# Kernel optimization log

Measured on AMD Instinct MI355X. Metric: run time of the kernel, lower is better.

The kernel has to match this reference:

```python
import jax, jax.numpy as jnp
import numpy as np

N = 20000      # nodes
D_IN = 512     # input_dim
D_H = 256      # hyper_dim = input_dim // 2
C = 7          # class_num
E = 320000     # edges per class graph
E2 = 100000    # candidate pair list length
B = 8192       # batch of evaluated pairs (edge_id)
H3 = D_IN + C * D_H  # 2304, GatedNetwork / fc2 width
MIN = 1e-15
CURV = 1.0

def _norm(x):
    return jnp.maximum(jnp.linalg.norm(x, axis=-1, keepdims=True), MIN)

def artanh(x):
    x = jnp.clip(x, -1.0 + 1e-7, 1.0 - 1e-7)
    return 0.5 * (jnp.log1p(x) - jnp.log1p(-x))

def proj(x, c):
    # clip to inside the Poincare ball
    n = _norm(x)
    maxn = (1.0 - 4e-3) / jnp.sqrt(c)
    return jnp.where(n > maxn, x / n * maxn, x)

def expmap0(u, c):
    sc = jnp.sqrt(c); n = _norm(u)
    return jnp.tanh(sc * n) * u / (sc * n)

def logmap0(p, c):
    sc = jnp.sqrt(c); n = _norm(p)
    return artanh(sc * n) * p / (sc * n)

def mobius_add(x, y, c):
    x2 = jnp.sum(x * x, -1, keepdims=True)
    y2 = jnp.sum(y * y, -1, keepdims=True)
    xy = jnp.sum(x * y, -1, keepdims=True)
    num = (1 + 2 * c * xy + c * y2) * x + (1 - c * x2) * y
    den = 1 + 2 * c * xy + c * c * x2 * y2
    return num / jnp.maximum(den, MIN)

def mobius_matvec(m, x, c):
    sc = jnp.sqrt(c)
    xn = _norm(x)
    mx = x @ m.T
    mxn = _norm(mx)
    res = jnp.tanh(mxn / xn * artanh(sc * xn)) * mx / (mxn * sc)
    zero = jnp.all(mx == 0, axis=-1, keepdims=True)
    return jnp.where(zero, jnp.zeros((), mx.dtype), res)


def setup_inputs() -> dict:
    key = jax.random.key(0)
    ks = iter(jax.random.split(key, 48))
    def dense(shape, fan_in):
        return jax.random.normal(next(ks), shape, jnp.float32) * (1.0 / np.sqrt(fan_in))
    inp = {}
    inp['f1'] = jax.random.normal(next(ks), (N, D_IN), jnp.float32)
    inp['adj_src'] = jax.random.randint(next(ks), (C, E), 0, N)
    inp['adj_dst'] = jax.random.randint(next(ks), (C, E), 0, N)
    inp['adj_val'] = jax.random.uniform(next(ks), (C, E), jnp.float32) / 16.0  # ~row-normalized weights
    inp['edge_src'] = jax.random.randint(next(ks), (C, E), 0, N)
    inp['edge_dst'] = jax.random.randint(next(ks), (C, E), 0, N)
    inp['edge_index'] = jax.random.randint(next(ks), (2, E2), 0, N)
    inp['edge_id'] = jax.random.randint(next(ks), (B,), 0, E2)
    # per-class HypLinear
    inp['W_hyp'] = dense((C, D_H, D_IN), D_IN)
    inp['b_hyp'] = jnp.zeros((C, D_H), jnp.float32)
    # per-class HyperbolicDecoder linear
    inp['Wd'] = dense((C, D_H, D_H), D_H)
    inp['bd'] = jnp.zeros((C, D_H), jnp.float32)
    # per-class GIN MLP: lin1 -> BN -> tanh -> lin2
    inp['Wg1'] = dense((C, D_H, D_H), D_H)
    inp['bg1'] = jnp.zeros((C, D_H), jnp.float32)
    inp['gamma'] = jnp.ones((C, D_H), jnp.float32)
    inp['beta'] = jnp.zeros((C, D_H), jnp.float32)
    inp['Wg2'] = dense((C, D_H, D_H), D_H)
    inp['bg2'] = jnp.zeros((C, D_H), jnp.float32)
    # GatedInteractionNetwork
    inp['Wgate'] = dense((H3, H3), H3); inp['bgate'] = jnp.zeros((H3,), jnp.float32)
    inp['Wint'] = dense((H3, H3), H3); inp['bint'] = jnp.zeros((H3,), jnp.float32)
    inp['Wout'] = dense((H3, H3), H3); inp['bout'] = jnp.zeros((H3,), jnp.float32)
    # fc2 MLP head
    inp['Wf1'] = dense((H3 // 2, H3), H3); inp['bf1'] = jnp.zeros((H3 // 2,), jnp.float32)
    inp['Wf2'] = dense((H3 // 4, H3 // 2), H3 // 2); inp['bf2'] = jnp.zeros((H3 // 4,), jnp.float32)
    inp['Wf3'] = dense((C, H3 // 4), H3 // 4); inp['bf3'] = jnp.zeros((C,), jnp.float32)
    return inp


def reference(f1, adj_val, W_hyp, b_hyp, Wd, bd, Wg1, bg1, gamma, beta, Wg2, bg2,
              Wgate, bgate, Wint, bint, Wout, bout, Wf1, bf1, Wf2, bf2, Wf3, bf3,
              adj_src, adj_dst, edge_src, edge_dst, edge_index, edge_id):
    c = jnp.float32(CURV)
    # proj_tan0 is identity on the Poincare ball
    x_hyp = proj(expmap0(f1, c), c)
    outs = [f1]
    for i in range(C):
        # HypLinear: mobius matvec + hyperbolic bias
        res = proj(mobius_matvec(W_hyp[i], x_hyp, c), c)
        hb = proj(expmap0(b_hyp[i][None, :], c), c)
        res = proj(mobius_add(res, hb, c), c)
        # HypAgg: spmm(adj, logmap0(x)) then expmap0
        xt = logmap0(res, c)                     # [N, D_H]
        msg = adj_val[i][:, None] * xt[adj_src[i]]
        support = jax.ops.segment_sum(msg, adj_dst[i], num_segments=N)
        h = proj(expmap0(support, c), c)
        # HypAct: relu in tangent space at origin
        h = proj(expmap0(jax.nn.relu(logmap0(h, c)), c), c)
        # HyperbolicDecoder: logmap0 then euclidean linear
        d = logmap0(h, c) @ Wd[i].T + bd[i]
        # GIN (1 layer, eps=0): mlp(x + sum_neighbors x_j), mlp = lin->BN->tanh->lin
        agg = d + jax.ops.segment_sum(d[edge_src[i]], edge_dst[i], num_segments=N)
        z = agg @ Wg1[i].T + bg1[i]
        mu = jnp.mean(z, axis=0)
        var = jnp.var(z, axis=0)
        z = (z - mu) / jnp.sqrt(var + 1e-5) * gamma[i] + beta[i]
        z = jnp.tanh(z)
        outs.append(z @ Wg2[i].T + bg2[i])
    x = jnp.concatenate(outs, axis=1)            # [N, H3]
    nid = edge_index[:, edge_id]                 # [2, B]
    x1 = x[nid[0]]
    x2 = x[nid[1]]
    # GatedInteractionNetwork
    gate = jax.nn.sigmoid((x1 + x2) @ Wgate.T + bgate)
    gi = gate * jax.nn.relu((x1 * x2) @ Wint.T + bint)
    g = gi @ Wout.T + bout
    # fc2 head
    h1 = jax.nn.relu(g @ Wf1.T + bf1)
    h2 = jax.nn.relu(h1 @ Wf2.T + bf2)
    return h2 @ Wf3.T + bf3                      # [B, C]
```

## Files before the change

### kernel.cpp

```cpp
#include <hip/hip_runtime.h>
#include <math.h>

#define N_NODES 20000
#define D_INN   512
#define DH      256
#define NCH     7
#define NE      320000
#define NE2     100000
#define NB      8192
#define H3      2304
#define MAXN    0.996f
#define LOG2E   1.44269504f

typedef unsigned short u16;
typedef __attribute__((ext_vector_type(8))) short bf16x8;
typedef __attribute__((ext_vector_type(4))) float f32x4;

__device__ __forceinline__ u16 f2b(float f) {
    unsigned int x = __float_as_uint(f);
    unsigned int r = (x + 0x7fffu + ((x >> 16) & 1u)) >> 16;
    return (u16)r;
}
__device__ __forceinline__ float b2f(u16 u) {
    return __uint_as_float(((unsigned int)u) << 16);
}
__device__ __forceinline__ float blo(unsigned int u) { return __uint_as_float(u << 16); }
__device__ __forceinline__ float bhi(unsigned int u) { return __uint_as_float(u & 0xffff0000u); }
__device__ __forceinline__ unsigned int pk2(float a, float b) {
    return (unsigned int)f2b(a) | ((unsigned int)f2b(b) << 16);
}

__device__ __forceinline__ float rcp_f(float x) { return __builtin_amdgcn_rcpf(x); }
__device__ __forceinline__ float exp2_f(float x) { return __builtin_amdgcn_exp2f(x); }
__device__ __forceinline__ float log2_f(float x) { return __builtin_amdgcn_logf(x); }
__device__ __forceinline__ float tanh_fast(float x) {
    float xc = fminf(fmaxf(x, -15.f), 15.f);
    float t = exp2_f(xc * (2.f * LOG2E));
    return (t - 1.f) * rcp_f(t + 1.f);
}
__device__ __forceinline__ float artanh_fast(float x) {
    x = fminf(fmaxf(x, -1.0f + 1e-7f), 1.0f - 1e-7f);
    return 0.34657359f * log2_f((1.f + x) * rcp_f(1.f - x));
}
__device__ __forceinline__ float sigmoid_fast(float x) {
    return rcp_f(1.f + exp2_f(-x * LOG2E));
}

__device__ __forceinline__ float wave_sum(float v) {
    #pragma unroll
    for (int off = 32; off > 0; off >>= 1) v += __shfl_xor(v, off, 64);
    return v;
}

__device__ __forceinline__ float block_sum256(float v) {
    __shared__ float sred[4];
    #pragma unroll
    for (int off = 32; off > 0; off >>= 1) v += __shfl_down(v, off, 64);
    int lane = threadIdx.x & 63;
    int w = threadIdx.x >> 6;
    if (lane == 0) sred[w] = v;
    __syncthreads();
    float tot = sred[0] + sred[1] + sred[2] + sred[3];
    __syncthreads();
    return tot;
}

__global__ void k_zero(float* __restrict__ p, int n) {
    int i = blockIdx.x * 256 + threadIdx.x;
    if (i < n) p[i] = 0.0f;
}
__global__ void k_izero(int* __restrict__ p, int n) {
    int i = blockIdx.x * 256 + threadIdx.x;
    if (i < n) p[i] = 0;
}

__global__ void k_f2b(const float* __restrict__ s, u16* __restrict__ d, int n4) {
    int i = blockIdx.x * 256 + threadIdx.x;
    int stride = gridDim.x * 256;
    for (; i < n4; i += stride) {
        float4 v = ((const float4*)s)[i];
        uint2 o; o.x = pk2(v.x, v.y); o.y = pk2(v.z, v.w);
        ((uint2*)d)[i] = o;
    }
}

__global__ void k_bias2(const float* __restrict__ a, const float* __restrict__ b,
                        float* __restrict__ o) {
    int i = blockIdx.x * 256 + threadIdx.x;
    if (i < H3) o[i] = a[i];
    else if (i < 2 * H3) o[i] = b[i - H3];
}

__global__ void k_gi(const u16* __restrict__ gate, const u16* __restrict__ tmp,
                     u16* __restrict__ out, int total4) {
    int i = blockIdx.x * 256 + threadIdx.x;
    int stride = gridDim.x * 256;
    for (; i < total4; i += stride) {
        uint2 g = ((const uint2*)gate)[i];
        uint2 t = ((const uint2*)tmp)[i];
        uint2 o;
        o.x = pk2(blo(g.x) * fmaxf(blo(t.x), 0.f), bhi(g.x) * fmaxf(bhi(t.x), 0.f));
        o.y = pk2(blo(g.y) * fmaxf(blo(t.y), 0.f), bhi(g.y) * fmaxf(bhi(t.y), 0.f));
        ((uint2*)out)[i] = o;
    }
}

__global__ void k_twd(const float* __restrict__ Wd, u16* __restrict__ Wdt) {
    __shared__ float tile[16][17];
    int z = blockIdx.z;
    int bx = blockIdx.x * 16, by = blockIdx.y * 16;
    int tx = threadIdx.x & 15, ty = threadIdx.x >> 4;
    tile[ty][tx] = Wd[(size_t)z * DH * DH + (size_t)(by + ty) * DH + bx + tx];
    __syncthreads();
    Wdt[(size_t)z * DH * DH + (size_t)(bx + ty) * DH + by + tx] = f2b(tile[tx][ty]);
}

__global__ void k_tr(const float* __restrict__ Win, u16* __restrict__ Wt) {
    __shared__ float tile[16][17];
    int bx = blockIdx.x * 16, by = blockIdx.y * 16;
    int tx = threadIdx.x & 15, ty = threadIdx.x >> 4;
    tile[ty][tx] = Win[(size_t)(by + ty) * H3 + bx + tx];
    __syncthreads();
    Wt[(size_t)(bx + ty) * H3 + by + tx] = f2b(tile[tx][ty]);
}

__global__ void k_bvec(const float* __restrict__ Wf1, const float* __restrict__ bout,
                       const float* __restrict__ bf1, float* __restrict__ bcomb) {
    int r = blockIdx.x * 4 + (threadIdx.x >> 6);
    int lane = threadIdx.x & 63;
    const float* row = Wf1 + (size_t)r * H3;
    float s = 0.f;
    for (int j = lane; j < H3; j += 64) s = fmaf(row[j], bout[j], s);
    s = wave_sum(s);
    if (lane == 0) bcomb[r] = s + bf1[r];
}

__global__ void k_cvec(const float* __restrict__ Wg1, const float* __restrict__ bd,
                       float* __restrict__ cvec) {
    int z = blockIdx.x, j = threadIdx.x;
    const float* row = Wg1 + (size_t)z * DH * DH + (size_t)j * DH;
    const float* b = bd + (size_t)z * DH;
    float s = 0.f;
    for (int k = 0; k < DH; ++k) s = fmaf(row[k], b[k], s);
    cvec[(size_t)z * DH + j] = s;
}

__global__ void k_hist2(const int* __restrict__ adjd, const int* __restrict__ edged,
                        int* __restrict__ cnt, int G) {
    int z = blockIdx.y;
    const int* dst = (z < G) ? adjd + (size_t)z * NE : edged + (size_t)(z - G) * NE;
    cnt += (size_t)z * N_NODES;
    int i = blockIdx.x * 256 + threadIdx.x;
    if (i < NE) atomicAdd(&cnt[dst[i]], 1);
}

__global__ void k_scan(int* __restrict__ cnt, int* __restrict__ rowptr) {
    int z = blockIdx.x;
    cnt += (size_t)z * N_NODES;
    rowptr += (size_t)z * (N_NODES + 1);
    __shared__ int part[256];
    int t = threadIdx.x;
    const int CH = (N_NODES + 255) / 256;
    int beg = t * CH;
    int end = beg + CH; if (end > N_NODES) end = N_NODES;
    int s = 0;
    for (int i = beg; i < end; ++i) s += cnt[i];
    part[t] = s;
    __syncthreads();
    for (int off = 1; off < 256; off <<= 1) {
        int v = (t >= off) ? part[t - off] : 0;
        __syncthreads();
        part[t] += v;
        __syncthreads();
    }
    int run = (t == 0) ? 0 : part[t - 1];
    for (int i = beg; i < end; ++i) {
        int c = cnt[i];
        rowptr[i] = run;
        cnt[i] = run;
        run += c;
    }
    if (t == 255) rowptr[N_NODES] = part[255];
}

__global__ void k_place2(const int* __restrict__ adjs, const int* __restrict__ adjd,
                         const float* __restrict__ adjv, const int* __restrict__ edges,
                         const int* __restrict__ edged, int* __restrict__ cursor,
                         uint2* __restrict__ padj, int* __restrict__ psrcE, int G) {
    int z = blockIdx.y;
    bool isadj = z < G;
    const int* src = isadj ? adjs + (size_t)z * NE : edges + (size_t)(z - G) * NE;
    const int* dst = isadj ? adjd + (size_t)z * NE : edged + (size_t)(z - G) * NE;
    cursor += (size_t)z * N_NODES;
    int i = blockIdx.x * 256 + threadIdx.x;
    if (i < NE) {
        int d = dst[i];
        int pos = atomicAdd(&cursor[d], 1);
        if (isadj) {
            uint2 p;
            p.x = (unsigned int)src[i];
            p.y = __float_as_uint(adjv[(size_t)z * NE + i]);
            padj[(size_t)z * NE + pos] = p;
        } else {
            psrcE[(size_t)(z - G) * NE + pos] = src[i];
        }
    }
}

__global__ void k_expmap_proj_in(const float* __restrict__ f1,
                                 u16* __restrict__ xhyp, float* __restrict__ xhn) {
    int r = blockIdx.x, t = threadIdx.x;
    const float* u = f1 + (size_t)r * D_INN;
    float v0 = u[t], v1 = u[t + 256];
    float ss = block_sum256(v0 * v0 + v1 * v1);
    float nraw = sqrtf(ss);
    float n = fmaxf(nraw, 1e-15f);
    float c = tanh_fast(n) * rcp_f(n);
    float ny = c * nraw;
    float np = fmaxf(ny, 1e-15f);
    float s = (np > MAXN) ? MAXN * rcp_f(np) : 1.0f;
    float cs = c * s;
    u16* o = xhyp + (size_t)r * D_INN;
    o[t] = f2b(cs * v0);
    o[t + 256] = f2b(cs * v1);
    if (t == 0) xhn[r] = fminf(np, MAXN);
}

__global__ void k_hb(const float* __restrict__ b_hyp,
                     float* __restrict__ hb, float* __restrict__ hb2) {
    int i = blockIdx.x, t = threadIdx.x;
    float v = b_hyp[i * DH + t];
    float ss = block_sum256(v * v);
    float nraw = sqrtf(ss);
    float n = fmaxf(nraw, 1e-15f);
    float c = tanh_fast(n) * rcp_f(n);
    float ny = c * nraw;
    float np = fmaxf(ny, 1e-15f);
    float s = (np > MAXN) ? MAXN * rcp_f(np) : 1.0f;
    float hv = c * s * v;
    hb[i * DH + t] = hv;
    float s2 = block_sum256(hv * hv);
    if (t == 0) hb2[i] = s2;
}

__global__ void k_rowfuse1(u16* __restrict__ T, const float* __restrict__ xhn,
                           const float* __restrict__ hb, const float* __restrict__ hb2) {
    int z = blockIdx.y;
    int n = blockIdx.x * 4 + (threadIdx.x >> 6);
    int lane = threadIdx.x & 63;
    u16* row = T + ((size_t)z * N_NODES + n) * DH;
    const float* hbz = hb + (size_t)z * DH;
    uint2 u = *(const uint2*)(row + lane * 4);
    float m0 = blo(u.x), m1 = bhi(u.x), m2 = blo(u.y), m3 = bhi(u.y);
    float ss = wave_sum(m0 * m0 + m1 * m1 + m2 * m2 + m3 * m3);
    float mxn_raw = sqrtf(ss);
    float mxn = fmaxf(mxn_raw, 1e-15f);
    float xn = xhn[n];
    float tt = tanh_fast(mxn * rcp_f(xn) * artanh_fast(xn));
    float coef = tt * rcp_f(mxn);
    float nres = coef * mxn_raw;
    float np = fmaxf(nres, 1e-15f);
    float s1 = (np > MAXN) ? MAXN * rcp_f(np) : 1.0f;
    float cs = coef * s1;
    float r0 = cs * m0, r1 = cs * m1, r2 = cs * m2, r3 = cs * m3;
    float n1 = fminf(np, MAXN);
    float4 hv = *(const float4*)(hbz + lane * 4);
    float xy = wave_sum(r0 * hv.x + r1 * hv.y + r2 * hv.z + r3 * hv.w);
    float x2 = n1 * n1, y2 = hb2[z];
    float ca = 1.0f + 2.0f * xy + y2;
    float cb = 1.0f - x2;
    float rden = rcp_f(fmaxf(1.0f + 2.0f * xy + x2 * y2, 1e-15f));
    float o0 = (ca * r0 + cb * hv.x) * rden;
    float o1 = (ca * r1 + cb * hv.y) * rden;
    float o2 = (ca * r2 + cb * hv.z) * rden;
    float o3 = (ca * r3 + cb * hv.w) * rden;
    float no2 = wave_sum(o0 * o0 + o1 * o1 + o2 * o2 + o3 * o3);
    float nop = fmaxf(sqrtf(no2), 1e-15f);
    float s2 = (nop > MAXN) ? MAXN * rcp_f(nop) : 1.0f;
    float n2 = fminf(nop, MAXN);
    float fin = artanh_fast(n2) * rcp_f(n2) * s2;
    uint2 o; o.x = pk2(fin * o0, fin * o1); o.y = pk2(fin * o2, fin * o3);
    *(uint2*)(row + lane * 4) = o;
}

__global__ void k_gather_fuse2(const int* __restrict__ rowptr, const uint2* __restrict__ padj,
                               const u16* __restrict__ xt, u16* __restrict__ out) {
    int z = blockIdx.y;
    rowptr += (size_t)z * (N_NODES + 1);
    padj += (size_t)z * NE;
    xt += (size_t)z * N_NODES * DH;
    out += (size_t)z * N_NODES * DH;
    int n = blockIdx.x * 4 + (threadIdx.x >> 6);
    int lane = threadIdx.x & 63;
    int beg = rowptr[n], end = rowptr[n + 1];
    float a0 = 0.f, a1 = 0.f, a2 = 0.f, a3 = 0.f;
    float b0 = 0.f, b1 = 0.f, b2 = 0.f, b3 = 0.f;
    int i = beg;
    for (; i + 2 <= end; i += 2) {
        uint2 p0 = padj[i];
        uint2 p1 = padj[i + 1];
        uint2 x0 = *(const uint2*)(xt + (size_t)p0.x * DH + lane * 4);
        uint2 x1 = *(const uint2*)(xt + (size_t)p1.x * DH + lane * 4);
        float v0 = __uint_as_float(p0.y), v1 = __uint_as_float(p1.y);
        a0 = fmaf(v0, blo(x0.x), a0);
        a1 = fmaf(v0, bhi(x0.x), a1);
        a2 = fmaf(v0, blo(x0.y), a2);
        a3 = fmaf(v0, bhi(x0.y), a3);
        b0 = fmaf(v1, blo(x1.x), b0);
        b1 = fmaf(v1, bhi(x1.x), b1);
        b2 = fmaf(v1, blo(x1.y), b2);
        b3 = fmaf(v1, bhi(x1.y), b3);
    }
    if (i < end) {
        uint2 p = padj[i];
        uint2 x0 = *(const uint2*)(xt + (size_t)p.x * DH + lane * 4);
        float v = __uint_as_float(p.y);
        a0 = fmaf(v, blo(x0.x), a0);
        a1 = fmaf(v, bhi(x0.x), a1);
        a2 = fmaf(v, blo(x0.y), a2);
        a3 = fmaf(v, bhi(x0.y), a3);
    }
    a0 += b0; a1 += b1; a2 += b2; a3 += b3;
    float ss = wave_sum(a0 * a0 + a1 * a1 + a2 * a2 + a3 * a3);
    float nraw = sqrtf(ss);
    float n_ = fmaxf(nraw, 1e-15f);
    float c1 = tanh_fast(n_) * rcp_f(n_);
    float nh = c1 * nraw;
    float np1 = fmaxf(nh, 1e-15f);
    float s1 = (np1 > MAXN) ? MAXN * rcp_f(np1) : 1.0f;
    float n1 = fminf(np1, MAXN);
    float cu = artanh_fast(n1) * rcp_f(n1) * s1 * c1;
    float u0 = fmaxf(cu * a0, 0.f), u1 = fmaxf(cu * a1, 0.f);
    float u2 = fmaxf(cu * a2, 0.f), u3 = fmaxf(cu * a3, 0.f);
    float ss2 = wave_sum(u0 * u0 + u1 * u1 + u2 * u2 + u3 * u3);
    float n2raw = sqrtf(ss2);
    float n2 = fmaxf(n2raw, 1e-15f);
    float c3 = tanh_fast(n2) * rcp_f(n2);
    float ne = c3 * n2raw;
    float np3 = fmaxf(ne, 1e-15f);
    float s3 = (np3 > MAXN) ? MAXN * rcp_f(np3) : 1.0f;
    float n3 = fminf(np3, MAXN);
    float cf = artanh_fast(n3) * rcp_f(n3) * s3 * c3;
    uint2 o; o.x = pk2(cf * u0, cf * u1); o.y = pk2(cf * u2, cf * u3);
    *(uint2*)(out + (size_t)n * DH + lane * 4) = o;
}

__global__ void k_gather_add(const int* __restrict__ rowptr, const int* __restrict__ psrc,
                             const u16* __restrict__ d, u16* __restrict__ out) {
    int z = blockIdx.y;
    rowptr += (size_t)z * (N_NODES + 1);
    psrc += (size_t)z * NE;
    d += (size_t)z * N_NODES * DH;
    out += (size_t)z * N_NODES * DH;
    int n = blockIdx.x * 4 + (threadIdx.x >> 6);
    int lane = threadIdx.x & 63;
    int beg = rowptr[n], end = rowptr[n + 1];
    uint2 u0v = *(const uint2*)(d + (size_t)n * DH + lane * 4);
    float a0 = blo(u0v.x), a1 = bhi(u0v.x), a2 = blo(u0v.y), a3 = bhi(u0v.y);
    float b0 = 0.f, b1 = 0.f, b2 = 0.f, b3 = 0.f;
    int i = beg;
    for (; i + 2 <= end; i += 2) {
        int s0 = psrc[i], s1 = psrc[i + 1];
        uint2 x0 = *(const uint2*)(d + (size_t)s0 * DH + lane * 4);
        uint2 x1 = *(const uint2*)(d + (size_t)s1 * DH + lane * 4);
        a0 += blo(x0.x); a1 += bhi(x0.x); a2 += blo(x0.y); a3 += bhi(x0.y);
        b0 += blo(x1.x); b1 += bhi(x1.x); b2 += blo(x1.y); b3 += bhi(x1.y);
    }
    if (i < end) {
        int s0 = psrc[i];
        uint2 x0 = *(const uint2*)(d + (size_t)s0 * DH + lane * 4);
        a0 += blo(x0.x); a1 += bhi(x0.x); a2 += blo(x0.y); a3 += bhi(x0.y);
    }
    a0 += b0; a1 += b1; a2 += b2; a3 += b3;
    uint2 o; o.x = pk2(a0, a1); o.y = pk2(a2, a3);
    *(uint2*)(out + (size_t)n * DH + lane * 4) = o;
}

__global__ void k_colstats(const u16* __restrict__ zp,
                           float* __restrict__ csum, float* __restrict__ csq) {
    int z = blockIdx.y;
    zp += (size_t)z * N_NODES * DH;
    csum += (size_t)z * DH;
    csq += (size_t)z * DH;
    int t = threadIdx.x;
    int r0 = blockIdx.x * 100;
    float s = 0.0f, q = 0.0f;
    for (int r = r0; r < r0 + 100; ++r) {
        float v = b2f(zp[(size_t)r * DH + t]);
        s += v;
        q += v * v;
    }
    atomicAdd(&csum[t], s);
    atomicAdd(&csq[t], q);
}

__global__ void k_normtanh_v(u16* __restrict__ zp, const float* __restrict__ csum,
                             const float* __restrict__ csq, const float* __restrict__ gamma,
                             const float* __restrict__ beta, int total4) {
    const float inv_n = 1.0f / N_NODES;
    int i = blockIdx.x * 256 + threadIdx.x;
    int stride = gridDim.x * 256;
    for (; i < total4; i += stride) {
        int e0 = i * 4;
        int z = e0 / (N_NODES * DH);
        int j0 = e0 & (DH - 1);
        int zb = z * DH + j0;
        uint2 u = ((uint2*)zp)[i];
        float v[4] = {blo(u.x), bhi(u.x), blo(u.y), bhi(u.y)};
        #pragma unroll
        for (int k = 0; k < 4; ++k) {
            float mu = csum[zb + k] * inv_n;
            float var = csq[zb + k] * inv_n - mu * mu;
            float inv = __builtin_amdgcn_rsqf(var + 1e-5f);
            v[k] = tanh_fast((v[k] - mu) * inv * gamma[zb + k] + beta[zb + k]);
        }
        uint2 o; o.x = pk2(v[0], v[1]); o.y = pk2(v[2], v[3]);
        ((uint2*)zp)[i] = o;
    }
}

__global__ void k_pair0(const int* __restrict__ ei, const int* __restrict__ eid,
                        const float* __restrict__ f1, u16* __restrict__ S,
                        u16* __restrict__ P) {
    int b = blockIdx.x, t = threadIdx.x;
    int e = eid[b];
    int n0 = ei[e], n1 = ei[NE2 + e];
    float2 a = *(const float2*)(f1 + (size_t)n0 * D_INN + t * 2);
    float2 c = *(const float2*)(f1 + (size_t)n1 * D_INN + t * 2);
    ((unsigned int*)(S + (size_t)b * H3))[t] = pk2(a.x + c.x, a.y + c.y);
    ((unsigned int*)(P + (size_t)b * H3))[t] = pk2(a.x * c.x, a.y * c.y);
}

__global__ void k_gather_ch(const int* __restrict__ ei, const int* __restrict__ eid,
                            const u16* __restrict__ zch, u16* __restrict__ S,
                            u16* __restrict__ P, int col0base) {
    int z = blockIdx.y;
    const u16* zp = zch + (size_t)z * N_NODES * DH;
    int col0 = col0base + z * DH;
    int b = blockIdx.x * 4 + (threadIdx.x >> 6);
    int lane = threadIdx.x & 63;
    int e = eid[b];
    int n0 = ei[e], n1 = ei[NE2 + e];
    uint2 ua = *(const uint2*)(zp + (size_t)n0 * DH + lane * 4);
    uint2 ub = *(const uint2*)(zp + (size_t)n1 * DH + lane * 4);
    float a0 = blo(ua.x), a1 = bhi(ua.x), a2 = blo(ua.y), a3 = bhi(ua.y);
    float c0 = blo(ub.x), c1 = bhi(ub.x), c2 = blo(ub.y), c3 = bhi(ub.y);
    uint2 so; so.x = pk2(a0 + c0, a1 + c1); so.y = pk2(a2 + c2, a3 + c3);
    uint2 po; po.x = pk2(a0 * c0, a1 * c1); po.y = pk2(a2 * c2, a3 * c3);
    *(uint2*)(S + (size_t)b * H3 + col0 + lane * 4) = so;
    *(uint2*)(P + (size_t)b * H3 + col0 + lane * 4) = po;
}

__global__ void k_final(const u16* __restrict__ h2, const float* __restrict__ Wf3,
                        const float* __restrict__ bf3, float* __restrict__ out) {
    int r = blockIdx.x, t = threadIdx.x;
    const u16* hr = h2 + (size_t)r * 576;
    float acc[7] = {0, 0, 0, 0, 0, 0, 0};
    for (int cb = t; cb < 576; cb += 64) {
        float h = b2f(hr[cb]);
        #pragma unroll
        for (int o = 0; o < 7; ++o) acc[o] = fmaf(h, Wf3[o * 576 + cb], acc[o]);
    }
    #pragma unroll
    for (int o = 0; o < 7; ++o) {
        #pragma unroll
        for (int off = 32; off > 0; off >>= 1) acc[o] += __shfl_down(acc[o], off, 64);
    }
    if (t == 0) {
        #pragma unroll
        for (int o = 0; o < 7; ++o) out[(size_t)r * 7 + o] = acc[o] + bf3[o];
    }
}

template <int EP>
__global__ __launch_bounds__(256, 2) void k_gemm_mfma(
    const u16* __restrict__ A, const u16* __restrict__ W,
    const float* __restrict__ bias, void* __restrict__ outv,
    const int* __restrict__ rpe, const float* __restrict__ cvec,
    int M, int N, int K, size_t sA, size_t sW, size_t sC, int sBias) {
    __shared__ short As[8192];
    __shared__ short Ws[8192];
    const int gx = gridDim.x, gy = gridDim.y;
    const int plane = gx * gy;
    const int total = plane * gridDim.z;
    const int orig = (blockIdx.z * gy + blockIdx.y) * gx + blockIdx.x;
    const int q8 = total >> 3, r8 = total & 7, xcd = orig & 7;
    const int wg = (xcd < r8 ? xcd * (q8 + 1) : r8 * (q8 + 1) + (xcd - r8) * q8) + (orig >> 3);
    const int z = wg / plane;
    const int rem = wg - z * plane;
    const int row0 = (rem / gx) * 128, col0 = (rem % gx) * 128;
    A += (size_t)z * sA;
    W += (size_t)z * sW;
    const size_t zC = (size_t)z * sC;
    const int* rp = (EP == 7) ? rpe + (size_t)z * (N_NODES + 1) : nullptr;
    const float* cv = (EP == 7) ? cvec + (size_t)z * DH : nullptr;
    const int t = threadIdx.x;
    const int lane = t & 63;
    const int w = t >> 6;
    const int wr = w >> 1, wc = w & 1;
    const int sr8 = lane >> 3;
    const int csrc = (lane & 7) ^ sr8;
    int gr[4], gc[4];
    #pragma unroll
    for (int p = 0; p < 4; ++p) {
        int rb = w + p * 4;
        gr[p] = row0 + rb * 8 + sr8; if (gr[p] >= M) gr[p] = M - 1;
        gc[p] = col0 + rb * 8 + sr8; if (gc[p] >= N) gc[p] = N - 1;
    }
    const int fr = lane & 15, fq4 = lane >> 4;
    f32x4 acc[4][4] = {};
    for (int k0 = 0; k0 < K; k0 += 64) {
        #pragma unroll
        for (int p = 0; p < 4; ++p) {
            int rb = w + p * 4;
            __builtin_amdgcn_global_load_lds(
                (const __attribute__((address_space(1))) unsigned int*)(A + (size_t)gr[p] * K + k0 + csrc * 8),
                (__attribute__((address_space(3))) unsigned int*)(As + rb * 512), 16, 0, 0);
            __builtin_amdgcn_global_load_lds(
                (const __attribute__((address_space(1))) unsigned int*)(W + (size_t)gc[p] * K + k0 + csrc * 8),
                (__attribute__((address_space(3))) unsigned int*)(Ws + rb * 512), 16, 0, 0);
        }
        __syncthreads();
        bf16x8 af[4][2], bfr[4][2];
        #pragma unroll
        for (int m = 0; m < 4; ++m) {
            int ar = wr * 64 + m * 16 + fr;
            #pragma unroll
            for (int kk = 0; kk < 2; ++kk) {
                int q = kk * 4 + fq4;
                af[m][kk] = *(const bf16x8*)(As + ar * 64 + ((q ^ (ar & 7)) * 8));
            }
        }
        #pragma unroll
        for (int n = 0; n < 4; ++n) {
            int br = wc * 64 + n * 16 + fr;
            #pragma unroll
            for (int kk = 0; kk < 2; ++kk) {
                int q = kk * 4 + fq4;
                bfr[n][kk] = *(const bf16x8*)(Ws + br * 64 + ((q ^ (br & 7)) * 8));
            }
        }
        #pragma unroll
        for (int m = 0; m < 4; ++m)
            #pragma unroll
            for (int n = 0; n < 4; ++n)
                #pragma unroll
                for (int kk = 0; kk < 2; ++kk)
                    acc[m][n] = __builtin_amdgcn_mfma_f32_16x16x32_bf16(
                        af[m][kk], bfr[n][kk], acc[m][n], 0, 0, 0);
        __syncthreads();
    }
    const int cl = lane & 15, rh = (lane >> 4) * 4;
    #pragma unroll
    for (int m = 0; m < 4; ++m) {
        float indf[4];
        if (EP == 7) {
            #pragma unroll
            for (int r = 0; r < 4; ++r) {
                int row = row0 + wr * 64 + m * 16 + rh + r;
                if (row >= M) row = M - 1;
                indf[r] = 1.0f + (float)(rp[row + 1] - rp[row]);
            }
        }
        #pragma unroll
        for (int n = 0; n < 4; ++n) {
            int col = col0 + wc * 64 + n * 16 + cl;
            if (col >= N) continue;
            float bv = bias ? bias[z * sBias + col] : 0.0f;
            float cvc = (EP == 7) ? cv[col] : 0.0f;
            #pragma unroll
            for (int r = 0; r < 4; ++r) {
                int row = row0 + wr * 64 + m * 16 + rh + r;
                if (row >= M) continue;
                float v = acc[m][n][r] + bv;
                size_t idx = zC + (size_t)row * N + col;
                if (EP == 2) ((u16*)outv)[idx] = f2b(sigmoid_fast(v));
                if (EP == 3) ((u16*)outv)[idx] = f2b(fmaxf(v, 0.0f));
                if (EP == 5) ((u16*)outv)[idx] = f2b(v);
                if (EP == 6) ((float*)outv)[idx] = fmaxf(v, 0.0f);
                if (EP == 7) ((u16*)outv)[idx] = f2b(v + indf[r] * cvc);
                if (EP == 8) ((u16*)outv)[idx] = (z == 0) ? f2b(sigmoid_fast(v)) : f2b(v);
            }
        }
    }
}

static inline void gemm_b(int ep, const u16* A, const u16* W, const float* bias, void* out,
                          const int* rpe, const float* cvec,
                          int M, int N, int K, int Z,
                          size_t sA, size_t sW, size_t sC, int sBias, hipStream_t st) {
    dim3 g((N + 127) / 128, (M + 127) / 128, Z);
    switch (ep) {
        case 2: k_gemm_mfma<2><<<g, 256, 0, st>>>(A, W, bias, out, rpe, cvec, M, N, K, sA, sW, sC, sBias); break;
        case 3: k_gemm_mfma<3><<<g, 256, 0, st>>>(A, W, bias, out, rpe, cvec, M, N, K, sA, sW, sC, sBias); break;
        case 5: k_gemm_mfma<5><<<g, 256, 0, st>>>(A, W, bias, out, rpe, cvec, M, N, K, sA, sW, sC, sBias); break;
        case 6: k_gemm_mfma<6><<<g, 256, 0, st>>>(A, W, bias, out, rpe, cvec, M, N, K, sA, sW, sC, sBias); break;
        case 7: k_gemm_mfma<7><<<g, 256, 0, st>>>(A, W, bias, out, rpe, cvec, M, N, K, sA, sW, sC, sBias); break;
        case 8: k_gemm_mfma<8><<<g, 256, 0, st>>>(A, W, bias, out, rpe, cvec, M, N, K, sA, sW, sC, sBias); break;
    }
}

static inline void conv_w(const float* s, u16* d, size_t n, hipStream_t st) {
    int n4 = (int)(n / 4);
    int grid = (n4 + 255) / 256;
    if (grid > 2048) grid = 2048;
    k_f2b<<<grid, 256, 0, st>>>(s, d, n4);
}

extern "C" void kernel_launch(void* const* d_in, const int* in_sizes, int n_in, void* d_out,
                              int out_size, void* d_ws, size_t ws_size, hipStream_t stream) {
    const float* f1 = (const float*)d_in[0];
    const int* adj_src = (const int*)d_in[1];
    const int* adj_dst = (const int*)d_in[2];
    const float* adj_val = (const float*)d_in[3];
    const int* edge_src = (const int*)d_in[4];
    const int* edge_dst = (const int*)d_in[5];
    const int* edge_index = (const int*)d_in[6];
    const int* edge_id = (const int*)d_in[7];
    const float* W_hyp = (const float*)d_in[8];
    const float* b_hyp = (const float*)d_in[9];
    const float* Wd = (const float*)d_in[10];
    const float* bd = (const float*)d_in[11];
    const float* Wg1 = (const float*)d_in[12];
    const float* bg1 = (const float*)d_in[13];
    const float* gamma = (const float*)d_in[14];
    const float* beta = (const float*)d_in[15];
    const float* Wg2 = (const float*)d_in[16];
    const float* bg2 = (const float*)d_in[17];
    const float* Wgate = (const float*)d_in[18];
    const float* bgate = (const float*)d_in[19];
    const float* Wint = (const float*)d_in[20];
    const float* bint = (const float*)d_in[21];
    const float* Wout = (const float*)d_in[22];
    const float* bout = (const float*)d_in[23];
    const float* Wf1 = (const float*)d_in[24];
    const float* bf1 = (const float*)d_in[25];
    const float* Wf2 = (const float*)d_in[26];
    const float* bf2 = (const float*)d_in[27];
    const float* Wf3 = (const float*)d_in[28];
    const float* bf3 = (const float*)d_in[29];
    float* outp = (float*)d_out;

    const bool single = ws_size >= 253400000ull;
    const int ngroups = single ? 1 : 2;
    const int GM = single ? 7 : 4;
    int g0s[2] = {0, 4};
    int gns[2] = {GM, 3};

    char* base = (char*)d_ws;
    size_t off = 0;
    auto alloc = [&](size_t bytes) -> char* {
        char* p = base + off;
        off += (bytes + 255) & ~(size_t)255;
        return p;
    };
    u16* Whyp_b = (u16*)alloc((size_t)NCH * DH * D_INN * 2);
    u16* Wc_b   = (u16*)alloc((size_t)NCH * DH * DH * 2);
    u16* Wg1_b  = (u16*)alloc((size_t)NCH * DH * DH * 2);
    u16* Wg2_b  = (u16*)alloc((size_t)NCH * DH * DH * 2);
    u16* Wgate_b = (u16*)alloc((size_t)H3 * H3 * 2);
    u16* Wint_b  = (u16*)alloc((size_t)H3 * H3 * 2);
    u16* Wcomb_b = (u16*)alloc((size_t)1152 * H3 * 2);
    u16* Wf2_b   = (u16*)alloc((size_t)576 * 1152 * 2);
    u16* S_b = (u16*)alloc((size_t)NB * H3 * 2);
    u16* P_b = (u16*)alloc((size_t)NB * H3 * 2);
    const size_t NDB = (size_t)N_NODES * DH;
    u16* buf1 = (u16*)alloc((size_t)GM * NDB * 2);
    u16* buf2 = (u16*)alloc((size_t)GM * NDB * 2);
    u16* xhyp_b = single ? buf2 : (u16*)alloc((size_t)N_NODES * D_INN * 2);
    int* cntC; int* rowptrC; uint2* padjC; int* psrcE;
    if (single) {
        padjC = (uint2*)S_b;
        psrcE = (int*)((char*)S_b + (size_t)GM * NE * 8);
        cntC = (int*)P_b;
        rowptrC = (int*)((char*)P_b + (size_t)2 * GM * N_NODES * 4);
    } else {
        cntC = (int*)alloc((size_t)2 * GM * N_NODES * 4);
        rowptrC = (int*)alloc((size_t)2 * GM * (N_NODES + 1) * 4);
        padjC = (uint2*)alloc((size_t)GM * NE * 8);
        psrcE = (int*)alloc((size_t)GM * NE * 4);
    }
    float* xhn = (float*)alloc((size_t)N_NODES * 4);
    float* hb = (float*)alloc((size_t)NCH * DH * 4);
    float* hb2 = (float*)alloc(NCH * 4);
    float* csum = (float*)alloc((size_t)GM * DH * 4);
    float* csq = (float*)alloc((size_t)GM * DH * 4);
    float* cvec_d = (float*)alloc((size_t)NCH * DH * 4);
    float* bias2 = (float*)alloc((size_t)2 * H3 * 4);
    float* bcomb = (float*)alloc((size_t)1152 * 4);
    u16* WoutT_b = buf1;
    u16* Wf1_b = buf1 + (size_t)H3 * H3;
    u16* Wdt_b = Wf1_b + (size_t)1152 * H3;
    u16* GT = buf1;
    u16* h2b = buf2;

    const int EG = (NE + 255) / 256;

    conv_w(W_hyp, Whyp_b, (size_t)NCH * DH * D_INN, stream);
    conv_w(Wg1, Wg1_b, (size_t)NCH * DH * DH, stream);
    conv_w(Wg2, Wg2_b, (size_t)NCH * DH * DH, stream);
    conv_w(Wgate, Wgate_b, (size_t)H3 * H3, stream);
    conv_w(Wint, Wint_b, (size_t)H3 * H3, stream);
    conv_w(Wf1, Wf1_b, (size_t)1152 * H3, stream);
    conv_w(Wf2, Wf2_b, (size_t)576 * 1152, stream);
    k_bias2<<<(2 * H3 + 255) / 256, 256, 0, stream>>>(bgate, bint, bias2);
    k_twd<<<dim3(16, 16, NCH), 256, 0, stream>>>(Wd, Wdt_b);
    gemm_b(5, Wg1_b, Wdt_b, nullptr, Wc_b, nullptr, nullptr,
           DH, DH, DH, NCH, (size_t)DH * DH, (size_t)DH * DH, (size_t)DH * DH, 0, stream);
    k_cvec<<<NCH, 256, 0, stream>>>(Wg1, bd, cvec_d);
    k_tr<<<dim3(144, 144), 256, 0, stream>>>(Wout, WoutT_b);
    gemm_b(5, Wf1_b, WoutT_b, nullptr, Wcomb_b, nullptr, nullptr,
           1152, H3, H3, 1, 0, 0, 0, 0, stream);
    k_bvec<<<1152 / 4, 256, 0, stream>>>(Wf1, bout, bf1, bcomb);

    k_expmap_proj_in<<<N_NODES, 256, 0, stream>>>(f1, xhyp_b, xhn);
    k_hb<<<NCH, 256, 0, stream>>>(b_hyp, hb, hb2);
    if (!single) k_pair0<<<NB, 256, 0, stream>>>(edge_index, edge_id, f1, S_b, P_b);

    for (int gi = 0; gi < ngroups; ++gi) {
        const int g0 = g0s[gi], G = gns[gi];
        const size_t eoff = (size_t)g0 * NE;
        const int G2 = 2 * G;
        const int* rpE = rowptrC + (size_t)G * (N_NODES + 1);
        k_izero<<<(G2 * N_NODES + 255) / 256, 256, 0, stream>>>(cntC, G2 * N_NODES);
        k_hist2<<<dim3(EG, G2), 256, 0, stream>>>(adj_dst + eoff, edge_dst + eoff, cntC, G);
        k_scan<<<G2, 256, 0, stream>>>(cntC, rowptrC);
        k_place2<<<dim3(EG, G2), 256, 0, stream>>>(adj_src + eoff, adj_dst + eoff,
                                                   adj_val + eoff, edge_src + eoff,
                                                   edge_dst + eoff, cntC, padjC, psrcE, G);
        gemm_b(5, xhyp_b, Whyp_b + (size_t)g0 * DH * D_INN, nullptr, buf1, nullptr,
               nullptr, N_NODES, DH, D_INN, G, 0, (size_t)DH * D_INN, NDB, 0, stream);
        k_rowfuse1<<<dim3(N_NODES / 4, G), 256, 0, stream>>>(buf1, xhn, hb + g0 * DH, hb2 + g0);
        k_gather_fuse2<<<dim3(N_NODES / 4, G), 256, 0, stream>>>(rowptrC, padjC, buf1, buf2);
        k_gather_add<<<dim3(N_NODES / 4, G), 256, 0, stream>>>(rpE, psrcE, buf2, buf1);
        gemm_b(7, buf1, Wc_b + (size_t)g0 * DH * DH, bg1 + g0 * DH, buf2,
               rpE, cvec_d + (size_t)g0 * DH, N_NODES, DH, DH, G,
               NDB, (size_t)DH * DH, NDB, DH, stream);
        k_zero<<<(2 * GM * DH + 255) / 256, 256, 0, stream>>>(csum, 2 * GM * DH);
        k_colstats<<<dim3(200, G), 256, 0, stream>>>(buf2, csum, csq);
        {
            int total4 = (int)(G * NDB / 4);
            int blocks = (total4 + 255) / 256;
            if (blocks > 2048) blocks = 2048;
            k_normtanh_v<<<blocks, 256, 0, stream>>>(buf2, csum, csq, gamma + g0 * DH,
                                                     beta + g0 * DH, total4);
        }
        gemm_b(5, buf2, Wg2_b + (size_t)g0 * DH * DH, bg2 + g0 * DH, buf1, nullptr,
               nullptr, N_NODES, DH, DH, G, NDB, (size_t)DH * DH, NDB, DH, stream);
        if (!single)
            k_gather_ch<<<dim3(NB / 4, G), 256, 0, stream>>>(edge_index, edge_id, buf1,
                                                             S_b, P_b, D_INN + g0 * DH);
    }
    if (single) {
        k_pair0<<<NB, 256, 0, stream>>>(edge_index, edge_id, f1, S_b, P_b);
        k_gather_ch<<<dim3(NB / 4, 7), 256, 0, stream>>>(edge_index, edge_id, buf1,
                                                         S_b, P_b, D_INN);
    }

    gemm_b(8, S_b, Wgate_b, bias2, GT, nullptr, nullptr, NB, H3, H3, 2,
           (size_t)NB * H3, (size_t)H3 * H3, (size_t)NB * H3, H3, stream);
    {
        int total4 = NB * H3 / 4;
        int blocks = (total4 + 255) / 256;
        if (blocks > 2048) blocks = 2048;
        k_gi<<<blocks, 256, 0, stream>>>(GT, GT + (size_t)NB * H3, S_b, total4);
    }
    gemm_b(3, S_b, Wcomb_b, bcomb, buf1, nullptr, nullptr, NB, 1152, H3, 1, 0, 0, 0, 0, stream);
    gemm_b(3, buf1, Wf2_b, bf2, h2b, nullptr, nullptr, NB, 576, 1152, 1, 0, 0, 0, 0, stream);
    k_final<<<NB, 64, 0, stream>>>(h2b, Wf3, bf3, outp);
}
```

Measured before the change: 1.601 ms.

## Replace scatter CSR placement with two-pass bucketed binning for locality

Replaces the single-pass per-edge global atomic scatter into CSR arrays with a two-stage approach when everything fits in one group. Edges are first binned into 40 coarse destination buckets using shared-memory histograms and one global atomic per bucket per block, writing packed src/dst into scratch space. A second kernel then places each bucket's edges into their final CSR slots using shared-memory cursors. This aims to cut scattered global atomics and random writes, at the cost of an extra scratch pass and more memory traffic.

```diff
diff --git a/kernel.cpp b/kernel.cpp
--- a/kernel.cpp
+++ b/kernel.cpp
@@ -11,6 +11,8 @@
 #define H3      2304
 #define MAXN    0.996f
 #define LOG2E   1.44269504f
+#define NBUK    40
+#define BSH     9
 
 typedef unsigned short u16;
 typedef __attribute__((ext_vector_type(8))) short bf16x8;
@@ -203,6 +205,91 @@
             padj[(size_t)z * NE + pos] = p;
         } else {
             psrcE[(size_t)(z - G) * NE + pos] = src[i];
+        }
+    }
+}
+
+__global__ void k_bcur(const int* __restrict__ rowptr, int* __restrict__ bcur, int G2) {
+    int i = blockIdx.x * 256 + threadIdx.x;
+    if (i < G2 * NBUK) {
+        int z = i / NBUK, b = i - z * NBUK;
+        bcur[i] = rowptr[(size_t)z * (N_NODES + 1) + (b << BSH)];
+    }
+}
+
+__global__ void k_binA(const int* __restrict__ adjs, const int* __restrict__ adjd,
+                       const float* __restrict__ adjv, const int* __restrict__ edges,
+                       const int* __restrict__ edged, int* __restrict__ bcur,
+                       uint2* __restrict__ scrA, unsigned int* __restrict__ scrE, int G) {
+    int z = blockIdx.y;
+    bool isadj = z < G;
+    const int* src = isadj ? adjs + (size_t)z * NE : edges + (size_t)(z - G) * NE;
+    const int* dst = isadj ? adjd + (size_t)z * NE : edged + (size_t)(z - G) * NE;
+    __shared__ int hcnt[NBUK];
+    __shared__ int gbase[NBUK];
+    int t = threadIdx.x;
+    int i = blockIdx.x * 256 + t;
+    if (t < NBUK) hcnt[t] = 0;
+    __syncthreads();
+    int s = 0, d = 0, buk = 0, rank = 0;
+    bool valid = i < NE;
+    if (valid) {
+        s = src[i]; d = dst[i];
+        buk = d >> BSH;
+        rank = atomicAdd(&hcnt[buk], 1);
+    }
+    __syncthreads();
+    if (t < NBUK && hcnt[t] > 0)
+        gbase[t] = atomicAdd(&bcur[z * NBUK + t], hcnt[t]);
+    __syncthreads();
+    if (valid) {
+        int pos = gbase[buk] + rank;
+        unsigned int sd = (unsigned int)s | ((unsigned int)d << 15);
+        if (isadj) {
+            uint2 p; p.x = sd; p.y = __float_as_uint(adjv[(size_t)z * NE + i]);
+            scrA[(size_t)z * NE + pos] = p;
+        } else {
+            scrE[(size_t)(z - G) * NE + pos] = sd;
+        }
+    }
+}
+
+__global__ void k_placeB(const int* __restrict__ rowptr, const uint2* __restrict__ scrA,
+                         const unsigned int* __restrict__ scrE, uint2* __restrict__ padj,
+                         int* __restrict__ psrcE, int G) {
+    int z = blockIdx.y;
+    int b = blockIdx.x;
+    bool isadj = z < G;
+    const int* rp = rowptr + (size_t)z * (N_NODES + 1);
+    __shared__ int cur[512];
+    int t = threadIdx.x;
+    int n0 = b << BSH;
+    for (int k = t; k < 512; k += 256) {
+        int node = n0 + k;
+        cur[k] = (node < N_NODES) ? rp[node] : 0;
+    }
+    __syncthreads();
+    int beg = rp[n0];
+    int nend = n0 + 512; if (nend > N_NODES) nend = N_NODES;
+    int end = rp[nend];
+    if (isadj) {
+        const uint2* sc = scrA + (size_t)z * NE;
+        uint2* out = padj + (size_t)z * NE;
+        for (int i = beg + t; i < end; i += 256) {
+            uint2 p = sc[i];
+            int d = (int)((p.x >> 15) & 0x7fffu);
+            int pos = atomicAdd(&cur[d - n0], 1);
+            uint2 o; o.x = p.x & 0x7fffu; o.y = p.y;
+            out[pos] = o;
+        }
+    } else {
+        const unsigned int* sc = scrE + (size_t)(z - G) * NE;
+        int* out = psrcE + (size_t)(z - G) * NE;
+        for (int i = beg + t; i < end; i += 256) {
+            unsigned int p = sc[i];
+            int d = (int)((p >> 15) & 0x7fffu);
+            int pos = atomicAdd(&cur[d - n0], 1);
+            out[pos] = (int)(p & 0x7fffu);
         }
     }
 }
@@ -669,11 +756,16 @@
     u16* buf2 = (u16*)alloc((size_t)GM * NDB * 2);
     u16* xhyp_b = single ? buf2 : (u16*)alloc((size_t)N_NODES * D_INN * 2);
     int* cntC; int* rowptrC; uint2* padjC; int* psrcE;
+    uint2* scrA = nullptr; unsigned int* scrE = nullptr;
     if (single) {
         padjC = (uint2*)S_b;
         psrcE = (int*)((char*)S_b + (size_t)GM * NE * 8);
         cntC = (int*)P_b;
         rowptrC = (int*)((char*)P_b + (size_t)2 * GM * N_NODES * 4);
+        size_t rp_end = (size_t)2 * GM * N_NODES * 4 + (size_t)2 * GM * (N_NODES + 1) * 4;
+        rp_end = (rp_end + 63) & ~(size_t)63;
+        scrA = (uint2*)((char*)P_b + rp_end);
+        scrE = (unsigned int*)((char*)scrA + (size_t)GM * NE * 8);
     } else {
         cntC = (int*)alloc((size_t)2 * GM * N_NODES * 4);
         rowptrC = (int*)alloc((size_t)2 * GM * (N_NODES + 1) * 4);
@@ -688,6 +780,7 @@
     float* cvec_d = (float*)alloc((size_t)NCH * DH * 4);
     float* bias2 = (float*)alloc((size_t)2 * H3 * 4);
     float* bcomb = (float*)alloc((size_t)1152 * 4);
+    int* bcur = (int*)alloc((size_t)2 * NCH * NBUK * 4);
     u16* WoutT_b = buf1;
     u16* Wf1_b = buf1 + (size_t)H3 * H3;
     u16* Wdt_b = Wf1_b + (size_t)1152 * H3;
@@ -725,9 +818,19 @@
         k_izero<<<(G2 * N_NODES + 255) / 256, 256, 0, stream>>>(cntC, G2 * N_NODES);
         k_hist2<<<dim3(EG, G2), 256, 0, stream>>>(adj_dst + eoff, edge_dst + eoff, cntC, G);
         k_scan<<<G2, 256, 0, stream>>>(cntC, rowptrC);
-        k_place2<<<dim3(EG, G2), 256, 0, stream>>>(adj_src + eoff, adj_dst + eoff,
-                                                   adj_val + eoff, edge_src + eoff,
-                                                   edge_dst + eoff, cntC, padjC, psrcE, G);
+        if (single) {
+            k_bcur<<<(G2 * NBUK + 255) / 256, 256, 0, stream>>>(rowptrC, bcur, G2);
+            k_binA<<<dim3(EG, G2), 256, 0, stream>>>(adj_src, adj_dst, adj_val,
+                                                     edge_src, edge_dst, bcur,
+                                                     scrA, scrE, G);
+            k_placeB<<<dim3(NBUK, G2), 256, 0, stream>>>(rowptrC, scrA, scrE,
+                                                         padjC, psrcE, G);
+        } else {
+            k_place2<<<dim3(EG, G2), 256, 0, stream>>>(adj_src + eoff, adj_dst + eoff,
+                                                       adj_val + eoff, edge_src + eoff,
+                                                       edge_dst + eoff, cntC, padjC,
+                                                       psrcE, G);
+        }
         gemm_b(5, xhyp_b, Whyp_b + (size_t)g0 * DH * D_INN, nullptr, buf1, nullptr,
                nullptr, N_NODES, DH, D_INN, G, 0, (size_t)DH * D_INN, NDB, 0, stream);
         k_rowfuse1<<<dim3(N_NODES / 4, G), 256, 0, stream>>>(buf1, xhn, hb + g0 * DH, hb2 + g0);
```

Measured after the change: 1.527 ms. 4.6% less time.
